# Performance work log

Hardware: AMD Instinct MI355X
Metric: run time of the kernel (lower is better)

## Reference

```python
import jax, jax.numpy as jnp
import numpy as np

EPS = 1e-5

def layer_norm(x, gamma, beta):
    mu = jnp.mean(x, axis=-1, keepdims=True)
    var = jnp.mean(jnp.square(x - mu), axis=-1, keepdims=True)
    return (x - mu) * jax.lax.rsqrt(var + EPS) * gamma + beta

def setup_inputs() -> dict:
    key = jax.random.key(0)
    ks = jax.random.split(key, 10)
    B, I, H = 4096, 2048, 2048
    G = 4 * H
    s_ih = 1.0 / np.sqrt(I)
    s_hh = 1.0 / np.sqrt(H)
    b_ih = jax.random.uniform(ks[4], (G,), jnp.float32, -s_ih, s_ih)
    b_hh = jax.random.uniform(ks[5], (G,), jnp.float32, -s_hh, s_hh)
    # forget-gate bias init to 1.0 (slot [H:2H] per the torch code's chunk order)
    b_ih = b_ih.at[H:2*H].set(1.0)
    b_hh = b_hh.at[H:2*H].set(1.0)
    return {
        "x": jax.random.normal(ks[0], (B, I), jnp.float32),
        "h_prev": jax.random.normal(ks[1], (B, H), jnp.float32),
        "c_prev": jax.random.normal(ks[2], (B, H), jnp.float32),
        "W_ih": jax.random.normal(ks[3], (I, G), jnp.float32) * s_ih,
        "W_hh": jax.random.normal(ks[6], (H, G), jnp.float32) * s_hh,
        "b_ih": b_ih,
        "b_hh": b_hh,
        "g_x": jnp.ones((G,), jnp.float32),
        "beta_x": jnp.zeros((G,), jnp.float32),
        "g_c": jnp.ones((H,), jnp.float32),
        "beta_c": jnp.zeros((H,), jnp.float32),
        "g_h": jnp.ones((H,), jnp.float32),
        "beta_h": jnp.zeros((H,), jnp.float32),
    }

def reference(x, h_prev, c_prev, W_ih, W_hh, b_ih, b_hh, g_x, beta_x, g_c, beta_c, g_h, beta_h):
    gates_x = layer_norm(x @ W_ih + b_ih, g_x, beta_x)   # LN only on input-path gates
    gates = gates_x + (h_prev @ W_hh + b_hh)              # [B, 4H]
    i_g, f_g, gg, o_g = jnp.split(gates, 4, axis=1)
    i_t = jax.nn.sigmoid(i_g)
    f_t = jax.nn.sigmoid(f_g)
    g_t = jnp.tanh(gg)
    o_t = jax.nn.sigmoid(o_g)
    c_t = layer_norm(f_t * c_prev + i_t * g_t, g_c, beta_c)
    h_t = layer_norm(o_t * jnp.tanh(c_t), g_h, beta_h)
    return (h_t, c_t)
```

## Files before the change

kernel.cpp:

```cpp
#include <hip/hip_runtime.h>
#include <stdint.h>

typedef unsigned short ushort_t;
typedef __attribute__((ext_vector_type(8))) short short8;
typedef __attribute__((ext_vector_type(4))) float f32x4;
typedef __attribute__((ext_vector_type(4))) ushort_t u16x4;

#define M_ROWS 4096
#define K_DIM  2048
#define N_GATE 8192
#define H_DIM  2048

__device__ __forceinline__ ushort_t f2bf(float f) {
    uint32_t u = __float_as_uint(f);
    uint32_t r = (u + 0x7FFFu + ((u >> 16) & 1u)) >> 16;
    return (ushort_t)r;
}
__device__ __forceinline__ float bf2f(ushort_t b) {
    return __uint_as_float(((uint32_t)b) << 16);
}
__device__ __forceinline__ float sigf(float x) {
    return 1.0f / (1.0f + __expf(-x));
}
__device__ __forceinline__ float tanh_fast(float x) {
    float e = __expf(2.0f * x);
    return 1.0f - 2.0f / (e + 1.0f);
}

__global__ void cvt_f32_bf16(const float* __restrict__ in, ushort_t* __restrict__ out, int n) {
    int i = (blockIdx.x * blockDim.x + threadIdx.x) * 4;
    if (i >= n) return;
    float4 v = *(const float4*)(in + i);
    u16x4 o;
    o[0] = f2bf(v.x); o[1] = f2bf(v.y); o[2] = f2bf(v.z); o[3] = f2bf(v.w);
    *(u16x4*)(out + i) = o;
}

__global__ void transpose_cvt(const float* __restrict__ W, ushort_t* __restrict__ Wt,
                              int K, int N) {
    __shared__ float tile[32][33];
    int bn = blockIdx.x * 32;
    int bk = blockIdx.y * 32;
    int tx = threadIdx.x;
    int ty = threadIdx.y;
#pragma unroll
    for (int i = 0; i < 32; i += 8)
        tile[ty + i][tx] = W[(size_t)(bk + ty + i) * N + bn + tx];
    __syncthreads();
#pragma unroll
    for (int i = 0; i < 32; i += 8)
        Wt[(size_t)(bn + ty + i) * K + bk + tx] = f2bf(tile[tx][ty + i]);
}

#define BM 128
#define BN 128
#define BK 64

__global__ void gemm_bt_bf16(const ushort_t* __restrict__ A0, const ushort_t* __restrict__ B0,
                             ushort_t* __restrict__ C0,
                             const ushort_t* __restrict__ A1, const ushort_t* __restrict__ B1,
                             ushort_t* __restrict__ C1,
                             int M, int N, int K) {
    const ushort_t* A  = blockIdx.z ? A1 : A0;
    const ushort_t* Bt = blockIdx.z ? B1 : B0;
    ushort_t*       C  = blockIdx.z ? C1 : C0;

    __shared__ ushort_t lds[2 * BM * BK];
    ushort_t* As = lds;
    ushort_t* Bs = lds + BM * BK;

    const int t    = threadIdx.x;
    const int lane = t & 63;
    const int wid  = t >> 6;
    const int wm   = wid >> 1;
    const int wn   = wid & 1;
    const int l15  = lane & 15;
    const int l4   = lane >> 4;

    const int brow = blockIdx.y * BM;
    const int bcol = blockIdx.x * BN;

    const int srow = t >> 3;
    const int scol = (t & 7) * 8;
    const size_t a_base = (size_t)(brow + srow) * K + scol;
    const size_t b_base = (size_t)(bcol + srow) * K + scol;
    const int lds_woff = wid * 512;

    f32x4 acc[4][4];
#pragma unroll
    for (int m = 0; m < 4; ++m)
#pragma unroll
        for (int n = 0; n < 4; ++n)
            acc[m][n] = f32x4{0.f, 0.f, 0.f, 0.f};

    for (int kt = 0; kt < K; kt += BK) {
#pragma unroll
        for (int i = 0; i < 4; ++i) {
            __builtin_amdgcn_global_load_lds(
                (const __attribute__((address_space(1))) void*)(A + a_base + kt + (size_t)i * 32 * K),
                (__attribute__((address_space(3))) void*)(As + i * 2048 + lds_woff), 16, 0, 0);
            __builtin_amdgcn_global_load_lds(
                (const __attribute__((address_space(1))) void*)(Bt + b_base + kt + (size_t)i * 32 * K),
                (__attribute__((address_space(3))) void*)(Bs + i * 2048 + lds_woff), 16, 0, 0);
        }
        asm volatile("s_waitcnt vmcnt(0)" ::: "memory");
        __syncthreads();

#pragma unroll
        for (int kk = 0; kk < 2; ++kk) {
            short8 a[4], b[4];
#pragma unroll
            for (int m = 0; m < 4; ++m)
                a[m] = *(const short8*)&As[(wm * 64 + m * 16 + l15) * BK + kk * 32 + l4 * 8];
#pragma unroll
            for (int n = 0; n < 4; ++n)
                b[n] = *(const short8*)&Bs[(wn * 64 + n * 16 + l15) * BK + kk * 32 + l4 * 8];
#pragma unroll
            for (int m = 0; m < 4; ++m)
#pragma unroll
                for (int n = 0; n < 4; ++n)
                    acc[m][n] = __builtin_amdgcn_mfma_f32_16x16x32_bf16(a[m], b[n], acc[m][n], 0, 0, 0);
        }
        __syncthreads();
    }

#pragma unroll
    for (int m = 0; m < 4; ++m) {
        int crow0 = brow + wm * 64 + m * 16 + l4 * 4;
#pragma unroll
        for (int n = 0; n < 4; ++n) {
            int ccol = bcol + wn * 64 + n * 16 + l15;
#pragma unroll
            for (int r = 0; r < 4; ++r)
                C[(size_t)(crow0 + r) * N + ccol] = f2bf(acc[m][n][r]);
        }
    }
}

__device__ __forceinline__ void block_reduce2(float& a, float& b, float* sred, int t) {
#pragma unroll
    for (int o = 32; o; o >>= 1) {
        a += __shfl_down(a, o);
        b += __shfl_down(b, o);
    }
    __syncthreads();
    if ((t & 63) == 0) { int w = t >> 6; sred[w] = a; sred[4 + w] = b; }
    __syncthreads();
    a = sred[0] + sred[1] + sred[2] + sred[3];
    b = sred[4] + sred[5] + sred[6] + sred[7];
}

__global__ __launch_bounds__(256) void fuse_ln_lstm(
    const ushort_t* __restrict__ xW, const ushort_t* __restrict__ hW,
    const float* __restrict__ c_prev,
    const float* __restrict__ b_ih, const float* __restrict__ b_hh,
    const float* __restrict__ g_x, const float* __restrict__ beta_x,
    const float* __restrict__ g_c, const float* __restrict__ beta_c,
    const float* __restrict__ g_h, const float* __restrict__ beta_h,
    float* __restrict__ h_out, float* __restrict__ c_out) {

    __shared__ float sgx[N_GATE];
    __shared__ float scell[H_DIM];
    __shared__ float sot[H_DIM];
    __shared__ float sred[8];

    const int b = blockIdx.x;
    const int t = threadIdx.x;
    const ushort_t* xwr = xW + (size_t)b * N_GATE;
    const ushort_t* hwr = hW + (size_t)b * N_GATE;
    const float*    cpr = c_prev + (size_t)b * H_DIM;

    float s = 0.f, q = 0.f;
#pragma unroll
    for (int it = 0; it < 4; ++it) {
        int idx = it * 2048 + t * 8;
        short8 v = *(const short8*)&xwr[idx];
#pragma unroll
        for (int j = 0; j < 8; ++j) {
            float f = bf2f((ushort_t)v[j]) + b_ih[idx + j];
            sgx[idx + j] = f;
            s += f; q += f * f;
        }
    }
    block_reduce2(s, q, sred, t);
    const float inv_g = 1.0f / (float)N_GATE;
    float mu   = s * inv_g;
    float rstd = rsqrtf(q * inv_g - mu * mu + 1e-5f);

    float cs = 0.f, cq = 0.f;
#pragma unroll
    for (int it = 0; it < 8; ++it) {
        int j = it * 256 + t;
        int ji = j, jf = j + 2048, jg = j + 4096, jo = j + 6144;
        float gi = (sgx[ji] - mu) * rstd * g_x[ji] + beta_x[ji] + bf2f(hwr[ji]) + b_hh[ji];
        float gf = (sgx[jf] - mu) * rstd * g_x[jf] + beta_x[jf] + bf2f(hwr[jf]) + b_hh[jf];
        float gg = (sgx[jg] - mu) * rstd * g_x[jg] + beta_x[jg] + bf2f(hwr[jg]) + b_hh[jg];
        float go = (sgx[jo] - mu) * rstd * g_x[jo] + beta_x[jo] + bf2f(hwr[jo]) + b_hh[jo];
        float i_t = sigf(gi);
        float f_t = sigf(gf);
        float g_t = tanh_fast(gg);
        float o_t = sigf(go);
        float cell = f_t * cpr[j] + i_t * g_t;
        scell[j] = cell;
        sot[j]   = o_t;
        cs += cell; cq += cell * cell;
    }
    block_reduce2(cs, cq, sred, t);
    const float inv_h = 1.0f / (float)H_DIM;
    float muc   = cs * inv_h;
    float rstdc = rsqrtf(cq * inv_h - muc * muc + 1e-5f);

    float hs = 0.f, hq = 0.f;
#pragma unroll
    for (int it = 0; it < 8; ++it) {
        int j = it * 256 + t;
        float ct = (scell[j] - muc) * rstdc * g_c[j] + beta_c[j];
        c_out[(size_t)b * H_DIM + j] = ct;
        float hp = sot[j] * tanh_fast(ct);
        sgx[j] = hp;
        hs += hp; hq += hp * hp;
    }
    block_reduce2(hs, hq, sred, t);
    float muh   = hs * inv_h;
    float rstdh = rsqrtf(hq * inv_h - muh * muh + 1e-5f);

#pragma unroll
    for (int it = 0; it < 8; ++it) {
        int j = it * 256 + t;
        h_out[(size_t)b * H_DIM + j] = (sgx[j] - muh) * rstdh * g_h[j] + beta_h[j];
    }
}

extern "C" void kernel_launch(void* const* d_in, const int* in_sizes, int n_in,
                              void* d_out, int out_size, void* d_ws, size_t ws_size,
                              hipStream_t stream) {
    const float* x      = (const float*)d_in[0];
    const float* h_prev = (const float*)d_in[1];
    const float* c_prev = (const float*)d_in[2];
    const float* W_ih   = (const float*)d_in[3];
    const float* W_hh   = (const float*)d_in[4];
    const float* b_ih   = (const float*)d_in[5];
    const float* b_hh   = (const float*)d_in[6];
    const float* g_x    = (const float*)d_in[7];
    const float* beta_x = (const float*)d_in[8];
    const float* g_c    = (const float*)d_in[9];
    const float* beta_c = (const float*)d_in[10];
    const float* g_h    = (const float*)d_in[11];
    const float* beta_h = (const float*)d_in[12];

    const int M = M_ROWS, K = K_DIM, N = N_GATE;

    ushort_t* Xb   = (ushort_t*)d_ws;
    ushort_t* Hb   = Xb   + (size_t)M * K;
    ushort_t* WihT = Hb   + (size_t)M * K;
    ushort_t* WhhT = WihT + (size_t)N * K;
    ushort_t* xWb  = WhhT + (size_t)N * K;
    ushort_t* hWb  = xWb  + (size_t)M * N;

    const int n_xh = M * K;
    cvt_f32_bf16<<<n_xh / (256 * 4), 256, 0, stream>>>(x,      Xb, n_xh);
    cvt_f32_bf16<<<n_xh / (256 * 4), 256, 0, stream>>>(h_prev, Hb, n_xh);

    transpose_cvt<<<dim3(N / 32, K / 32), dim3(32, 8), 0, stream>>>(W_ih, WihT, K, N);
    transpose_cvt<<<dim3(N / 32, K / 32), dim3(32, 8), 0, stream>>>(W_hh, WhhT, K, N);

    gemm_bt_bf16<<<dim3(N / BN, M / BM, 2), 256, 0, stream>>>(
        Xb, WihT, xWb, Hb, WhhT, hWb, M, N, K);

    float* h_out = (float*)d_out;
    float* c_out = h_out + (size_t)M * H_DIM;
    fuse_ln_lstm<<<M, 256, 0, stream>>>(xWb, hWb, c_prev, b_ih, b_hh,
                                        g_x, beta_x, g_c, beta_c, g_h, beta_h,
                                        h_out, c_out);
}
```

Baseline: 420.2 us.

## Replace bf16 GEMM with 256x256 tile, 8-phase double-buffered pipelined kernel

```diff
diff --git a/kernel.cpp b/kernel.cpp
--- a/kernel.cpp
+++ b/kernel.cpp
@@ -52,89 +52,125 @@
         Wt[(size_t)(bn + ty + i) * K + bk + tx] = f2bf(tile[tx][ty + i]);
 }
 
-#define BM 128
-#define BN 128
-#define BK 64
-
-__global__ void gemm_bt_bf16(const ushort_t* __restrict__ A0, const ushort_t* __restrict__ B0,
-                             ushort_t* __restrict__ C0,
-                             const ushort_t* __restrict__ A1, const ushort_t* __restrict__ B1,
-                             ushort_t* __restrict__ C1,
-                             int M, int N, int K) {
+#define TBK 64
+
+__global__ __launch_bounds__(512, 2) void gemm256_8ph(
+    const ushort_t* __restrict__ A0, const ushort_t* __restrict__ B0, ushort_t* __restrict__ C0,
+    const ushort_t* __restrict__ A1, const ushort_t* __restrict__ B1, ushort_t* __restrict__ C1,
+    int M, int N, int K) {
+    extern __shared__ char smem[];
     const ushort_t* A  = blockIdx.z ? A1 : A0;
     const ushort_t* Bt = blockIdx.z ? B1 : B0;
     ushort_t*       C  = blockIdx.z ? C1 : C0;
 
-    __shared__ ushort_t lds[2 * BM * BK];
-    ushort_t* As = lds;
-    ushort_t* Bs = lds + BM * BK;
-
     const int t    = threadIdx.x;
-    const int lane = t & 63;
-    const int wid  = t >> 6;
-    const int wm   = wid >> 1;
-    const int wn   = wid & 1;
+    const int lane = t & 63, wid = t >> 6;
+    const int wm   = wid >> 2, wn = wid & 3;
     const int l15  = lane & 15;
-    const int l4   = lane >> 4;
-
-    const int brow = blockIdx.y * BM;
-    const int bcol = blockIdx.x * BN;
+    const int l4c  = (lane >> 4) * 16;
+
+    const int brow = blockIdx.y * 256;
+    const int bcol = blockIdx.x * 256;
 
     const int srow = t >> 3;
-    const int scol = (t & 7) * 8;
-    const size_t a_base = (size_t)(brow + srow) * K + scol;
-    const size_t b_base = (size_t)(bcol + srow) * K + scol;
-    const int lds_woff = wid * 512;
-
-    f32x4 acc[4][4];
-#pragma unroll
-    for (int m = 0; m < 4; ++m)
-#pragma unroll
-        for (int n = 0; n < 4; ++n)
-            acc[m][n] = f32x4{0.f, 0.f, 0.f, 0.f};
-
-    for (int kt = 0; kt < K; kt += BK) {
-#pragma unroll
-        for (int i = 0; i < 4; ++i) {
-            __builtin_amdgcn_global_load_lds(
-                (const __attribute__((address_space(1))) void*)(A + a_base + kt + (size_t)i * 32 * K),
-                (__attribute__((address_space(3))) void*)(As + i * 2048 + lds_woff), 16, 0, 0);
-            __builtin_amdgcn_global_load_lds(
-                (const __attribute__((address_space(1))) void*)(Bt + b_base + kt + (size_t)i * 32 * K),
-                (__attribute__((address_space(3))) void*)(Bs + i * 2048 + lds_woff), 16, 0, 0);
+    const int scol = ((t & 7) * 8) ^ (((t >> 5) & 1) * 16);
+    const ushort_t* gA = A  + (size_t)(brow + srow) * K + scol;
+    const ushort_t* gB = Bt + (size_t)(bcol + srow) * K + scol;
+    const int ldsw = wid * 1024;
+
+    int aR[4], abit[4], bR[2], bbit[2];
+#pragma unroll
+    for (int fm = 0; fm < 4; ++fm) { int r = wm * 64 + fm * 16 + l15; aR[fm] = r * 128; abit[fm] = ((r >> 2) & 1) << 5; }
+#pragma unroll
+    for (int fn = 0; fn < 2; ++fn) { int r = wn * 32 + fn * 16 + l15; bR[fn] = r * 128; bbit[fn] = ((r >> 2) & 1) << 5; }
+
+    f32x4 acc[8][4];
+#pragma unroll
+    for (int i = 0; i < 8; ++i)
+#pragma unroll
+        for (int j = 0; j < 4; ++j) acc[i][j] = f32x4{0.f, 0.f, 0.f, 0.f};
+
+    short8 a[4][2], b0[2][2], b1[2][2];
+
+#define STAGE_A(tt, h, buf) { _Pragma("unroll") for (int j = 0; j < 2; ++j) \
+    __builtin_amdgcn_global_load_lds( \
+        (const __attribute__((address_space(1))) void*)(gA + ((size_t)((h) * 128 + j * 64)) * K + (size_t)(tt) * TBK), \
+        (__attribute__((address_space(3))) void*)(smem + (buf) * 65536 + (h) * 16384 + j * 8192 + ldsw), 16, 0, 0); }
+#define STAGE_B(tt, h, buf) { _Pragma("unroll") for (int j = 0; j < 2; ++j) \
+    __builtin_amdgcn_global_load_lds( \
+        (const __attribute__((address_space(1))) void*)(gB + ((size_t)((h) * 128 + j * 64)) * K + (size_t)(tt) * TBK), \
+        (__attribute__((address_space(3))) void*)(smem + 32768 + (buf) * 65536 + (h) * 16384 + j * 8192 + ldsw), 16, 0, 0); }
+#define LDA(mh, buf) { _Pragma("unroll") for (int fm = 0; fm < 4; ++fm) _Pragma("unroll") for (int ks = 0; ks < 2; ++ks) \
+    a[fm][ks] = *(const short8*)(smem + (buf) * 65536 + (mh) * 16384 + aR[fm] + ((ks * 64 + l4c) ^ abit[fm])); }
+#define LDB(dst, nh, buf) { _Pragma("unroll") for (int fn = 0; fn < 2; ++fn) _Pragma("unroll") for (int ks = 0; ks < 2; ++ks) \
+    dst[fn][ks] = *(const short8*)(smem + 32768 + (buf) * 65536 + (nh) * 16384 + bR[fn] + ((ks * 64 + l4c) ^ bbit[fn])); }
+#define BARRIER() __builtin_amdgcn_s_barrier()
+#define LGKM0()  { asm volatile("s_waitcnt lgkmcnt(0)" ::: "memory"); __builtin_amdgcn_sched_barrier(0); }
+#define VM6()    asm volatile("s_waitcnt vmcnt(6)" ::: "memory")
+#define MM(mh, nh, bb) { __builtin_amdgcn_s_setprio(1); \
+    _Pragma("unroll") for (int ks = 0; ks < 2; ++ks) \
+    _Pragma("unroll") for (int fm = 0; fm < 4; ++fm) \
+    _Pragma("unroll") for (int fn = 0; fn < 2; ++fn) \
+        acc[(mh) * 4 + fm][(nh) * 2 + fn] = __builtin_amdgcn_mfma_f32_16x16x32_bf16( \
+            a[fm][ks], bb[fn][ks], acc[(mh) * 4 + fm][(nh) * 2 + fn], 0, 0, 0); \
+    __builtin_amdgcn_s_setprio(0); }
+
+    STAGE_A(0, 0, 0); STAGE_B(0, 0, 0); STAGE_B(0, 1, 0); STAGE_A(0, 1, 0);
+    STAGE_A(1, 0, 1); STAGE_B(1, 0, 1); STAGE_B(1, 1, 1);
+    VM6();
+    BARRIER();
+
+    const int NT = K / TBK;
+    for (int tt = 0; tt < NT; tt += 2) {
+        const int s2 = (tt + 2) & (NT - 1);
+        const int s3 = (tt + 3) & (NT - 1);
+        LDA(0, 0); LDB(b0, 0, 0);
+        STAGE_A(tt + 1, 1, 1);
+        BARRIER(); LGKM0(); MM(0, 0, b0); BARRIER();
+        LDB(b1, 1, 0);
+        STAGE_A(s2, 0, 0);
+        BARRIER(); LGKM0(); MM(0, 1, b1); BARRIER();
+        LDA(1, 0);
+        STAGE_B(s2, 0, 0);
+        BARRIER(); LGKM0(); MM(1, 0, b0); BARRIER();
+        STAGE_B(s2, 1, 0);
+        VM6();
+        BARRIER(); LGKM0(); MM(1, 1, b1); BARRIER();
+        LDA(0, 1); LDB(b0, 0, 1);
+        STAGE_A(s2, 1, 0);
+        BARRIER(); LGKM0(); MM(0, 0, b0); BARRIER();
+        LDB(b1, 1, 1);
+        STAGE_A(s3, 0, 1);
+        BARRIER(); LGKM0(); MM(0, 1, b1); BARRIER();
+        LDA(1, 1);
+        STAGE_B(s3, 0, 1);
+        BARRIER(); LGKM0(); MM(1, 0, b0); BARRIER();
+        STAGE_B(s3, 1, 1);
+        VM6();
+        BARRIER(); LGKM0(); MM(1, 1, b1); BARRIER();
+    }
+
+#pragma unroll
+    for (int i = 0; i < 8; ++i) {
+        const int mh = i >> 2, fm = i & 3;
+        const int row0 = brow + mh * 128 + wm * 64 + fm * 16 + (lane >> 4) * 4;
+#pragma unroll
+        for (int jn = 0; jn < 4; ++jn) {
+            const int nh = jn >> 1, fn = jn & 1;
+            const int col = bcol + nh * 128 + wn * 32 + fn * 16 + l15;
+#pragma unroll
+            for (int r = 0; r < 4; ++r)
+                C[(size_t)(row0 + r) * N + col] = f2bf(acc[i][jn][r]);
         }
-        asm volatile("s_waitcnt vmcnt(0)" ::: "memory");
-        __syncthreads();
-
-#pragma unroll
-        for (int kk = 0; kk < 2; ++kk) {
-            short8 a[4], b[4];
-#pragma unroll
-            for (int m = 0; m < 4; ++m)
-                a[m] = *(const short8*)&As[(wm * 64 + m * 16 + l15) * BK + kk * 32 + l4 * 8];
-#pragma unroll
-            for (int n = 0; n < 4; ++n)
-                b[n] = *(const short8*)&Bs[(wn * 64 + n * 16 + l15) * BK + kk * 32 + l4 * 8];
-#pragma unroll
-            for (int m = 0; m < 4; ++m)
-#pragma unroll
-                for (int n = 0; n < 4; ++n)
-                    acc[m][n] = __builtin_amdgcn_mfma_f32_16x16x32_bf16(a[m], b[n], acc[m][n], 0, 0, 0);
-        }
-        __syncthreads();
-    }
-
-#pragma unroll
-    for (int m = 0; m < 4; ++m) {
-        int crow0 = brow + wm * 64 + m * 16 + l4 * 4;
-#pragma unroll
-        for (int n = 0; n < 4; ++n) {
-            int ccol = bcol + wn * 64 + n * 16 + l15;
-#pragma unroll
-            for (int r = 0; r < 4; ++r)
-                C[(size_t)(crow0 + r) * N + ccol] = f2bf(acc[m][n][r]);
-        }
-    }
+    }
+#undef STAGE_A
+#undef STAGE_B
+#undef LDA
+#undef LDB
+#undef BARRIER
+#undef LGKM0
+#undef VM6
+#undef MM
 }
 
 __device__ __forceinline__ void block_reduce2(float& a, float& b, float* sred, int t) {
@@ -264,7 +300,13 @@
     transpose_cvt<<<dim3(N / 32, K / 32), dim3(32, 8), 0, stream>>>(W_ih, WihT, K, N);
     transpose_cvt<<<dim3(N / 32, K / 32), dim3(32, 8), 0, stream>>>(W_hh, WhhT, K, N);
 
-    gemm_bt_bf16<<<dim3(N / BN, M / BM, 2), 256, 0, stream>>>(
+    static int lds_attr_set = 0;
+    if (!lds_attr_set) {
+        (void)hipFuncSetAttribute(reinterpret_cast<const void*>(&gemm256_8ph),
+                                  hipFuncAttributeMaxDynamicSharedMemorySize, 131072);
+        lds_attr_set = 1;
+    }
+    gemm256_8ph<<<dim3(N / 256, M / 256, 2), 512, 131072, stream>>>(
         Xb, WihT, xWb, Hb, WhhT, hWb, M, N, K);
 
     float* h_out = (float*)d_out;
```

After: 385.6 us. 1.09x faster.
